# Optimization experiments

Hardware: AMD Instinct MI355X
Metric: run time of the kernel (lower is better)

## Reference

```python
import jax, jax.numpy as jnp
import numpy as np

N_DIMS = 4
NEG_SLOPE = 0.01
ALPHA = 0.5

def leaky(v):
    return jnp.where(v > 0, v, NEG_SLOPE * v)

def gcn_conv(h, W, b, edge_index, n):
    """PyG GCNConv: add self-loops, symmetric normalization, then aggregate."""
    hw = h @ W  # [N, H]
    loops = jnp.arange(n, dtype=edge_index.dtype)
    src = jnp.concatenate([edge_index[0], loops])
    dst = jnp.concatenate([edge_index[1], loops])
    deg = jax.ops.segment_sum(jnp.ones_like(dst, dtype=hw.dtype), dst, num_segments=n)
    dinv = jnp.where(deg > 0, jax.lax.rsqrt(deg), 0.0)
    norm = dinv[src] * dinv[dst]  # [E+N]
    out = jax.ops.segment_sum(hw[src] * norm[:, None], dst, num_segments=n)
    return out + b

def setup_inputs() -> dict:
    key = jax.random.key(0)
    ks = jax.random.split(key, 8)
    N, IN, H, OUT, E = 50000, 512, 256, 512, 800000
    def kaiming(k, shape, fan_in):
        bound = np.sqrt(6.0 / fan_in)  # kaiming_uniform a=sqrt(5)-ish approx; gain sqrt(2)/sqrt(fan_in)*sqrt(3)
        bound = np.sqrt(2.0) * np.sqrt(3.0 / fan_in)
        return jax.random.uniform(k, shape, jnp.float32, -bound, bound)
    x = jax.random.normal(ks[0], (N, IN), jnp.float32)
    all_dim_edge_index = jax.random.randint(ks[1], (N_DIMS, 2, E), 0, N, jnp.int64)
    proj_mat = kaiming(ks[2], (N_DIMS, IN, H), IN)
    gcn_W = jax.random.uniform(ks[3], (N_DIMS, H, H), jnp.float32, -1, 1) * np.sqrt(1.0 / H)
    gcn_b = jnp.zeros((N_DIMS, H), jnp.float32)
    bilinear = kaiming(ks[4], (H, H), H)
    fan = H * N_DIMS
    inv_W = jax.random.uniform(ks[5], (fan, OUT), jnp.float32, -np.sqrt(1.0 / fan), np.sqrt(1.0 / fan))
    inv_b = jax.random.uniform(ks[6], (OUT,), jnp.float32, -np.sqrt(1.0 / fan), np.sqrt(1.0 / fan))
    return {"x": x, "all_dim_edge_index": all_dim_edge_index, "proj_mat": proj_mat,
            "gcn_W": gcn_W, "gcn_b": gcn_b, "bilinear": bilinear, "inv_W": inv_W, "inv_b": inv_b}

def reference(x, all_dim_edge_index, proj_mat, gcn_W, gcn_b, bilinear, inv_W, inv_b):
    n = x.shape[0]
    # per-dimension projection: [n_dims, N, H]
    dim_repr = leaky(jnp.einsum('ni,dih->dnh', x, proj_mat))
    # within-dimension GCN message passing (loop over small fixed n_dims)
    within_aggr = jnp.stack([
        gcn_conv(dim_repr[d], gcn_W[d], gcn_b[d], all_dim_edge_index[d], n)
        for d in range(N_DIMS)])
    # cross-dimension attention
    attention = jnp.einsum('aji,ik,bjk->ab', proj_mat, bilinear, proj_mat)
    attention = jax.nn.softmax(attention, axis=0)
    across_aggr = jnp.einsum('ab,anh->bnh', attention, dim_repr)
    new_dim_repr = ALPHA * within_aggr + (1.0 - ALPHA) * across_aggr  # [n_dims, N, H]
    concat = jnp.transpose(new_dim_repr, (1, 0, 2)).reshape(n, -1)  # [N, n_dims*H]
    return leaky(concat @ inv_W + inv_b)
```

## Files before the change

kernel.cpp:

```cpp
#include <hip/hip_runtime.h>
#include <math.h>

constexpr int N_NODES = 50000;
constexpr int IN_F    = 512;
constexpr int H_F     = 256;
constexpr int OUT_F   = 512;
constexpr int N_EDGE  = 800000;
constexpr int NDIM    = 4;
constexpr long NH     = (long)N_NODES * H_F;

#define LEAKY_SLOPE 0.01f

__device__ __forceinline__ float leaky_f(float v) { return v > 0.0f ? v : LEAKY_SLOPE * v; }

typedef __bf16 bf16x8 __attribute__((ext_vector_type(8)));
typedef float  f32x4  __attribute__((ext_vector_type(4)));

struct PtrTab { const __bf16* h[8]; const __bf16* l[8]; };

__device__ __forceinline__ void gload16(const void* g, void* s) {
  __builtin_amdgcn_global_load_lds(
      (const __attribute__((address_space(1))) void*)g,
      (__attribute__((address_space(3))) void*)s, 16, 0, 0);
}

template<bool AF32>
__global__ __launch_bounds__(256) void gemm_k(
    const float* __restrict__ Af, int ldaf,
    PtrTab at, int lda,
    const __bf16* __restrict__ BhT, const __bf16* __restrict__ BlT, int ldb,
    float* __restrict__ C, int ldc,
    const float* __restrict__ biasVec,
    __bf16* __restrict__ Oh, __bf16* __restrict__ Ol, int ldo,
    int M, int N, int K, int accumulate, int leaky)
{
  __shared__ __bf16 AshF[2][4096];
  __shared__ __bf16 AslF[2][4096];
  __shared__ __bf16 BshF[2][4096];
  __shared__ __bf16 BslF[2][4096];

  const int tid  = threadIdx.x;
  const int lane = tid & 63;
  const int wid  = tid >> 6;
  const int wm   = wid & 1;
  const int wn   = wid >> 1;
  const int l15  = lane & 15;
  const int quad = lane >> 4;

  const int nwg = (int)(gridDim.x * gridDim.y);
  const int hw  = (int)(blockIdx.y * gridDim.x + blockIdx.x);
  const int xcd = hw & 7, idx = hw >> 3;
  const int q8 = nwg >> 3, r8 = nwg & 7;
  const int wk = (xcd < r8 ? xcd * (q8 + 1) : r8 * (q8 + 1) + (xcd - r8) * q8) + idx;
  const int col0 = (wk % (int)gridDim.x) * 128;
  const int row0 = (wk / (int)gridDim.x) * 128;

  f32x4 acc[4][4] = {};
  const int nkt = K >> 5;

  float4 areg[4];

  auto stageB = [&](int buf, int kt) {
    const int kb = kt << 5;
    #pragma unroll
    for (int p = 0; p < 2; ++p) {
      const int c  = tid + p * 256;
      const int rr = c >> 2;
      const int sw = ((c & 3) ^ ((rr >> 1) & 3)) * 8;
      const size_t go = (size_t)(col0 + rr) * ldb + kb + sw;
      gload16(BhT + go, &BshF[buf][c * 8]);
      gload16(BlT + go, &BslF[buf][c * 8]);
    }
  };
  auto stageA = [&](int buf, int kt) {
    const int ch = kt >> 3;
    const __bf16* __restrict__ Ah = at.h[ch];
    const __bf16* __restrict__ Al = at.l[ch];
    const int ka = (kt & 7) << 5;
    #pragma unroll
    for (int p = 0; p < 2; ++p) {
      const int c  = tid + p * 256;
      const int rr = c >> 2;
      const int sw = ((c & 3) ^ ((rr >> 1) & 3)) * 8;
      int row = row0 + rr; row = row < M ? row : M - 1;
      const size_t go = (size_t)row * lda + ka + sw;
      gload16(Ah + go, &AshF[buf][c * 8]);
      gload16(Al + go, &AslF[buf][c * 8]);
    }
  };
  auto loadA32 = [&](int kt) {
    #pragma unroll
    for (int p = 0; p < 4; ++p) {
      const int m = (tid >> 3) + p * 32;
      int row = row0 + m; row = row < M ? row : M - 1;
      areg[p] = *(const float4*)(Af + (size_t)row * ldaf + (kt << 5) + (tid & 7) * 4);
    }
  };
  auto writeA32 = [&](int buf) {
    const int q16 = (tid & 7) >> 1;
    const int sub = (tid & 1) * 4;
    #pragma unroll
    for (int p = 0; p < 4; ++p) {
      const int m = (tid >> 3) + p * 32;
      const float f[4] = {areg[p].x, areg[p].y, areg[p].z, areg[p].w};
      union { __bf16 b[4]; short4 s; } hh, ll;
      #pragma unroll
      for (int i = 0; i < 4; ++i) {
        const __bf16 hb = (__bf16)f[i];
        hh.b[i] = hb;
        ll.b[i] = (__bf16)(f[i] - (float)hb);
      }
      const int off = m * 32 + ((q16 ^ ((m >> 1) & 3)) * 8) + sub;
      *(short4*)&AshF[buf][off] = hh.s;
      *(short4*)&AslF[buf][off] = ll.s;
    }
  };

  if constexpr (AF32) {
    loadA32(0);
    stageB(0, 0);
    writeA32(0);
  } else {
    stageA(0, 0);
    stageB(0, 0);
  }
  __syncthreads();

  int cur = 0;
  for (int kt = 0; kt < nkt; ++kt) {
    const bool more = (kt + 1 < nkt);
    if constexpr (AF32) {
      if (more) { loadA32(kt + 1); stageB(cur ^ 1, kt + 1); }
    } else {
      if (more) { stageA(cur ^ 1, kt + 1); stageB(cur ^ 1, kt + 1); }
    }

    bf16x8 ah[4], al[4], bh[4], bl[4];
    #pragma unroll
    for (int t = 0; t < 4; ++t) {
      const int ar = wm * 64 + t * 16 + l15;
      const int br = wn * 64 + t * 16 + l15;
      const int as = ar * 32 + ((quad ^ ((ar >> 1) & 3)) * 8);
      const int bs = br * 32 + ((quad ^ ((br >> 1) & 3)) * 8);
      ah[t] = *(const bf16x8*)&AshF[cur][as];
      al[t] = *(const bf16x8*)&AslF[cur][as];
      bh[t] = *(const bf16x8*)&BshF[cur][bs];
      bl[t] = *(const bf16x8*)&BslF[cur][bs];
    }
    #pragma unroll
    for (int mt = 0; mt < 4; ++mt)
      #pragma unroll
      for (int nt = 0; nt < 4; ++nt) {
        acc[mt][nt] = __builtin_amdgcn_mfma_f32_16x16x32_bf16(ah[mt], bh[nt], acc[mt][nt], 0, 0, 0);
        acc[mt][nt] = __builtin_amdgcn_mfma_f32_16x16x32_bf16(ah[mt], bl[nt], acc[mt][nt], 0, 0, 0);
        acc[mt][nt] = __builtin_amdgcn_mfma_f32_16x16x32_bf16(al[mt], bh[nt], acc[mt][nt], 0, 0, 0);
      }

    if constexpr (AF32) {
      if (more) writeA32(cur ^ 1);
    }
    __syncthreads();
    cur ^= 1;
  }

  #pragma unroll
  for (int mt = 0; mt < 4; ++mt)
    #pragma unroll
    for (int nt = 0; nt < 4; ++nt) {
      const int col = col0 + wn * 64 + nt * 16 + l15;
      const float bv = biasVec ? biasVec[col] : 0.0f;
      #pragma unroll
      for (int r = 0; r < 4; ++r) {
        const int row = row0 + wm * 64 + mt * 16 + quad * 4 + r;
        if (row < M) {
          float v = acc[mt][nt][r] + bv;
          if (accumulate) v += C[(size_t)row * ldc + col];
          if (leaky) v = leaky_f(v);
          if (Oh) {
            const __bf16 hv = (__bf16)v;
            Oh[(size_t)row * ldo + col] = hv;
            Ol[(size_t)row * ldo + col] = (__bf16)(v - (float)hv);
          } else {
            C[(size_t)row * ldc + col] = v;
          }
        }
      }
    }
}

__global__ void splitT_kernel(const float* __restrict__ B, __bf16* __restrict__ h,
                              __bf16* __restrict__ l, int Kd, int Nd, int total)
{
  int i = blockIdx.x * 256 + threadIdx.x;
  if (i >= total) return;
  int z   = i / (Kd * Nd);
  int rem = i - z * (Kd * Nd);
  int k = rem / Nd;
  int n = rem - k * Nd;
  float v = B[i];
  __bf16 hv = (__bf16)v;
  long o = (long)z * Kd * Nd + (long)n * Kd + k;
  h[o] = hv;
  l[o] = (__bf16)(v - (float)hv);
}

__global__ void splitA_kernel(const float* __restrict__ A, __bf16* __restrict__ h,
                              __bf16* __restrict__ l, long total)
{
  long i = (long)blockIdx.x * 256 + threadIdx.x;
  if (i >= total) return;
  float v = A[i];
  __bf16 hv = (__bf16)v;
  h[i] = hv;
  l[i] = (__bf16)(v - (float)hv);
}

__global__ void bcat_kernel(const float* __restrict__ invW, const float* __restrict__ att,
                            __bf16* __restrict__ h, __bf16* __restrict__ l)
{
  int i = blockIdx.x * 256 + threadIdx.x;
  if (i >= NDIM * OUT_F * 512) return;
  int d   = i >> 18;
  int rem = i & 262143;
  int n = rem >> 9;
  int k = rem & 511;
  float v;
  if (k < H_F) {
    v = invW[(long)(d * H_F + k) * OUT_F + n];
  } else {
    float s = 0.f;
    #pragma unroll
    for (int b = 0; b < 4; ++b)
      s += att[d * 4 + b] * invW[(long)(b * H_F + (k - H_F)) * OUT_F + n];
    v = 0.5f * s;
  }
  __bf16 hv = (__bf16)v;
  long o = (long)n * (NDIM * 512) + d * 512 + k;
  h[o] = hv;
  l[o] = (__bf16)(v - (float)hv);
}

__global__ void deg_count_kernel(const int* __restrict__ edges, int* __restrict__ cnt, int E)
{
  int i = blockIdx.x * 256 + threadIdx.x;
  if (i >= NDIM * E) return;
  int d = i / E;
  int e = i - d * E;
  int t = edges[(long)d * 2 * E + E + e];
  atomicAdd(&cnt[d * N_NODES + t], 1);
}

__global__ __launch_bounds__(1024) void scan_kernel(const int* __restrict__ cnt,
                                                    int* __restrict__ row_start,
                                                    float* __restrict__ dinv)
{
  const int d    = blockIdx.x;
  const int tid  = threadIdx.x;
  const int lane = tid & 63;
  const int wid  = tid >> 6;
  __shared__ int wsum[16];
  __shared__ int carry_s;
  if (tid == 0) carry_s = 0;
  __syncthreads();
  for (int base = 0; base < N_NODES; base += 1024) {
    int i = base + tid;
    int v = (i < N_NODES) ? cnt[d * N_NODES + i] : 0;
    if (i < N_NODES) dinv[d * N_NODES + i] = sqrtf(0.5f / (float)(v + 1));
    int incl = v;
    #pragma unroll
    for (int off = 1; off < 64; off <<= 1) {
      int nb = __shfl_up(incl, off, 64);
      if (lane >= off) incl += nb;
    }
    if (lane == 63) wsum[wid] = incl;
    __syncthreads();
    if (wid == 0 && lane < 16) {
      int s = wsum[lane];
      #pragma unroll
      for (int off = 1; off < 16; off <<= 1) {
        int nb = __shfl_up(s, off, 16);
        if (lane >= off) s += nb;
      }
      wsum[lane] = s;
    }
    __syncthreads();
    int waveoff = (wid == 0) ? 0 : wsum[wid - 1];
    if (i < N_NODES) row_start[d * (N_NODES + 1) + i] = carry_s + waveoff + incl - v;
    __syncthreads();
    if (tid == 1023) carry_s += wsum[15];
    __syncthreads();
  }
  if (tid == 0) row_start[d * (N_NODES + 1) + N_NODES] = carry_s;
}

__global__ void fill_kernel(const int* __restrict__ edges, const int* __restrict__ row_start,
                            int* __restrict__ fill_cnt, int* __restrict__ csr_src, int E)
{
  int i = blockIdx.x * 256 + threadIdx.x;
  if (i >= NDIM * E) return;
  int d = i / E;
  int e = i - d * E;
  int s = edges[(long)d * 2 * E + e];
  int t = edges[(long)d * 2 * E + E + e];
  int pos = row_start[d * (N_NODES + 1) + t] + atomicAdd(&fill_cnt[d * N_NODES + t], 1);
  csr_src[(long)d * E + pos] = s;
}

__global__ __launch_bounds__(256) void gather_aggr_kernel(
    const float* __restrict__ hw, const int* __restrict__ csr_src,
    const int* __restrict__ row_start, const float* __restrict__ dinv,
    const float* __restrict__ bias, __bf16* __restrict__ Wh, __bf16* __restrict__ Wl)
{
  const int n = blockIdx.x * 4 + (threadIdx.x >> 6);
  const int lane = threadIdx.x & 63;
  const float dt = dinv[n];
  const float sl = dt * dt;
  const float4 b = *(const float4*)(bias + lane * 4);
  const float4 h = *(const float4*)(hw + (size_t)n * H_F + lane * 4);
  float4 a0 = make_float4(0.5f * b.x + sl * h.x, 0.5f * b.y + sl * h.y,
                          0.5f * b.z + sl * h.z, 0.5f * b.w + sl * h.w);
  float4 a1 = make_float4(0.f, 0.f, 0.f, 0.f);
  const int beg = row_start[n];
  const int end = row_start[n + 1];
  int j = beg;
  for (; j + 2 <= end; j += 2) {
    const int s0 = csr_src[j];
    const int s1 = csr_src[j + 1];
    const float nm0 = dt * dinv[s0];
    const float nm1 = dt * dinv[s1];
    const float4 v0 = *(const float4*)(hw + (size_t)s0 * H_F + lane * 4);
    const float4 v1 = *(const float4*)(hw + (size_t)s1 * H_F + lane * 4);
    a0.x = fmaf(nm0, v0.x, a0.x); a0.y = fmaf(nm0, v0.y, a0.y);
    a0.z = fmaf(nm0, v0.z, a0.z); a0.w = fmaf(nm0, v0.w, a0.w);
    a1.x = fmaf(nm1, v1.x, a1.x); a1.y = fmaf(nm1, v1.y, a1.y);
    a1.z = fmaf(nm1, v1.z, a1.z); a1.w = fmaf(nm1, v1.w, a1.w);
  }
  if (j < end) {
    const int s0 = csr_src[j];
    const float nm0 = dt * dinv[s0];
    const float4 v0 = *(const float4*)(hw + (size_t)s0 * H_F + lane * 4);
    a0.x = fmaf(nm0, v0.x, a0.x); a0.y = fmaf(nm0, v0.y, a0.y);
    a0.z = fmaf(nm0, v0.z, a0.z); a0.w = fmaf(nm0, v0.w, a0.w);
  }
  const float av[4] = {a0.x + a1.x, a0.y + a1.y, a0.z + a1.z, a0.w + a1.w};
  union { __bf16 b[4]; short4 s; } H, L;
  #pragma unroll
  for (int i = 0; i < 4; ++i) {
    const __bf16 hv = (__bf16)av[i];
    H.b[i] = hv;
    L.b[i] = (__bf16)(av[i] - (float)hv);
  }
  *(short4*)(Wh + (size_t)n * H_F + lane * 4) = H.s;
  *(short4*)(Wl + (size_t)n * H_F + lane * 4) = L.s;
}

__global__ void att_dot_kernel(const float* __restrict__ T, const float* __restrict__ P,
                               float* __restrict__ out16)
{
  const int a = blockIdx.x >> 2;
  const int b = blockIdx.x & 3;
  const float* ta = T + (long)a * (IN_F * H_F);
  const float* pb = P + (long)b * (IN_F * H_F);
  float s = 0.f;
  for (int i = threadIdx.x; i < IN_F * H_F; i += 256) s += ta[i] * pb[i];
  #pragma unroll
  for (int off = 32; off > 0; off >>= 1) s += __shfl_down(s, off, 64);
  __shared__ float red[4];
  if ((threadIdx.x & 63) == 0) red[threadIdx.x >> 6] = s;
  __syncthreads();
  if (threadIdx.x == 0) out16[blockIdx.x] = red[0] + red[1] + red[2] + red[3];
}

__global__ void att_softmax_kernel(const float* __restrict__ raw, float* __restrict__ att)
{
  int b = threadIdx.x;
  if (b < 4) {
    float r0 = raw[b], r1 = raw[4 + b], r2 = raw[8 + b], r3 = raw[12 + b];
    float m = fmaxf(fmaxf(r0, r1), fmaxf(r2, r3));
    float e0 = expf(r0 - m), e1 = expf(r1 - m), e2 = expf(r2 - m), e3 = expf(r3 - m);
    float inv = 1.0f / (e0 + e1 + e2 + e3);
    att[b] = e0 * inv; att[4 + b] = e1 * inv; att[8 + b] = e2 * inv; att[12 + b] = e3 * inv;
  }
}

extern "C" void kernel_launch(void* const* d_in, const int* in_sizes, int n_in,
                              void* d_out, int out_size, void* d_ws, size_t ws_size,
                              hipStream_t stream)
{
  const float* x     = (const float*)d_in[0];
  const int*   edges = (const int*)d_in[1];
  const float* proj  = (const float*)d_in[2];
  const float* gcnW  = (const float*)d_in[3];
  const float* gcnB  = (const float*)d_in[4];
  const float* bil   = (const float*)d_in[5];
  const float* invW  = (const float*)d_in[6];
  const float* invB  = (const float*)d_in[7];
  float* out = (float*)d_out;

  float* HWB       = (float*)d_ws;
  float* dinv      = HWB + NH;
  float* Tbuf      = dinv + NDIM * N_NODES;
  float* att_raw   = Tbuf + (long)NDIM * IN_F * H_F;
  float* att       = att_raw + 16;
  int*   cnt       = (int*)(att + 16);
  int*   fill_cnt  = cnt + NDIM * N_NODES;
  int*   row_start = fill_cnt + NDIM * N_NODES;
  int*   csr_src   = row_start + NDIM * (N_NODES + 1);
  __bf16* projTh   = (__bf16*)(csr_src + (long)NDIM * N_EDGE);
  __bf16* projTl   = projTh + (long)NDIM * IN_F * H_F;
  __bf16* gcnWTh   = projTl + (long)NDIM * IN_F * H_F;
  __bf16* gcnWTl   = gcnWTh + (long)NDIM * H_F * H_F;
  __bf16* bcatTh   = gcnWTl + (long)NDIM * H_F * H_F;
  __bf16* bcatTl   = bcatTh + (long)NDIM * OUT_F * 512;
  __bf16* bilTh    = bcatTl + (long)NDIM * OUT_F * 512;
  __bf16* bilTl    = bilTh + (long)H_F * H_F;
  __bf16* dynBase  = bilTl + (long)H_F * H_F;

  const size_t base_bytes  = (size_t)((char*)dynBase - (char*)d_ws);
  const size_t need_merged = base_bytes + (size_t)16 * NH * sizeof(__bf16);
  const size_t need_xs     = need_merged + (size_t)2 * N_NODES * IN_F * sizeof(__bf16);
  const bool MERGED = ws_size >= need_merged;
  const bool XS     = ws_size >= need_xs;
  const int  RD     = MERGED ? NDIM : 1;

  __bf16* Rh  = dynBase;
  __bf16* Rl  = Rh + (long)RD * NH;
  __bf16* WBh = Rl + (long)RD * NH;
  __bf16* WBl = WBh + (long)RD * NH;
  __bf16* xh  = WBl + (long)RD * NH;
  __bf16* xl  = xh + (long)N_NODES * IN_F;

  const int MBL = (N_NODES + 127) / 128;
  PtrTab empty{};

  hipMemsetAsync(cnt, 0, (size_t)2 * NDIM * N_NODES * sizeof(int), stream);
  deg_count_kernel<<<(NDIM * N_EDGE + 255) / 256, 256, 0, stream>>>(edges, cnt, N_EDGE);
  scan_kernel<<<NDIM, 1024, 0, stream>>>(cnt, row_start, dinv);
  fill_kernel<<<(NDIM * N_EDGE + 255) / 256, 256, 0, stream>>>(edges, row_start, fill_cnt,
                                                               csr_src, N_EDGE);

  splitT_kernel<<<(NDIM * IN_F * H_F + 255) / 256, 256, 0, stream>>>(
      proj, projTh, projTl, IN_F, H_F, NDIM * IN_F * H_F);
  splitT_kernel<<<(NDIM * H_F * H_F + 255) / 256, 256, 0, stream>>>(
      gcnW, gcnWTh, gcnWTl, H_F, H_F, NDIM * H_F * H_F);
  splitT_kernel<<<(H_F * H_F + 255) / 256, 256, 0, stream>>>(
      bil, bilTh, bilTl, H_F, H_F, H_F * H_F);

  for (int a = 0; a < NDIM; ++a)
    gemm_k<true><<<dim3(H_F / 128, IN_F / 128), 256, 0, stream>>>(
        proj + (long)a * IN_F * H_F, H_F,
        empty, 0,
        bilTh, bilTl, H_F,
        Tbuf + (long)a * IN_F * H_F, H_F,
        nullptr, nullptr, nullptr, 0,
        IN_F, H_F, H_F, 0, 0);
  att_dot_kernel<<<16, 256, 0, stream>>>(Tbuf, proj, att_raw);
  att_softmax_kernel<<<1, 64, 0, stream>>>(att_raw, att);
  bcat_kernel<<<(NDIM * OUT_F * 512 + 255) / 256, 256, 0, stream>>>(invW, att, bcatTh, bcatTl);

  if (XS)
    splitA_kernel<<<(int)(((long)N_NODES * IN_F + 255) / 256), 256, 0, stream>>>(
        x, xh, xl, (long)N_NODES * IN_F);

  if (MERGED) {
    for (int d = 0; d < NDIM; ++d) {
      if (XS) {
        PtrTab t{};
        for (int c = 0; c < 8; ++c) { t.h[c] = xh + (c & 1) * 256; t.l[c] = xl + (c & 1) * 256; }
        gemm_k<false><<<dim3(H_F / 128, MBL), 256, 0, stream>>>(
            nullptr, 0, t, IN_F,
            projTh + (long)d * IN_F * H_F, projTl + (long)d * IN_F * H_F, IN_F,
            nullptr, 0, nullptr,
            Rh + (long)d * NH, Rl + (long)d * NH, H_F,
            N_NODES, H_F, IN_F, 0, 1);
      } else {
        gemm_k<true><<<dim3(H_F / 128, MBL), 256, 0, stream>>>(
            x, IN_F, empty, 0,
            projTh + (long)d * IN_F * H_F, projTl + (long)d * IN_F * H_F, IN_F,
            nullptr, 0, nullptr,
            Rh + (long)d * NH, Rl + (long)d * NH, H_F,
            N_NODES, H_F, IN_F, 0, 1);
      }
    }
  }

  for (int d = 0; d < NDIM; ++d) {
    const long rslot = MERGED ? d : 0;
    if (!MERGED) {
      gemm_k<true><<<dim3(H_F / 128, MBL), 256, 0, stream>>>(
          x, IN_F, empty, 0,
          projTh + (long)d * IN_F * H_F, projTl + (long)d * IN_F * H_F, IN_F,
          nullptr, 0, nullptr,
          Rh, Rl, H_F,
          N_NODES, H_F, IN_F, 0, 1);
    }
    {
      PtrTab t{};
      for (int c = 0; c < 8; ++c) { t.h[c] = Rh + rslot * NH; t.l[c] = Rl + rslot * NH; }
      gemm_k<false><<<dim3(H_F / 128, MBL), 256, 0, stream>>>(
          nullptr, 0, t, H_F,
          gcnWTh + (long)d * H_F * H_F, gcnWTl + (long)d * H_F * H_F, H_F,
          HWB, H_F, nullptr,
          nullptr, nullptr, 0,
          N_NODES, H_F, H_F, 0, 0);
    }
    gather_aggr_kernel<<<N_NODES / 4, 256, 0, stream>>>(
        HWB, csr_src + (long)d * N_EDGE, row_start + d * (N_NODES + 1),
        dinv + d * N_NODES, gcnB + d * H_F,
        WBh + rslot * NH, WBl + rslot * NH);

    if (!MERGED) {
      PtrTab t{};
      for (int c = 0; c < 8; ++c) {
        t.h[c] = (c & 1) ? Rh : WBh;
        t.l[c] = (c & 1) ? Rl : WBl;
      }
      gemm_k<false><<<dim3(OUT_F / 128, MBL), 256, 0, stream>>>(
          nullptr, 0, t, H_F,
          bcatTh + (long)d * 512, bcatTl + (long)d * 512, NDIM * 512,
          out, OUT_F, (d == 0) ? invB : nullptr,
          nullptr, nullptr, 0,
          N_NODES, OUT_F, 512, (d == 0) ? 0 : 1, (d == NDIM - 1) ? 1 : 0);
    }
  }

  if (MERGED) {
    PtrTab t{};
    for (int c = 0; c < 8; ++c) {
      const long dd = c >> 1;
      t.h[c] = (c & 1) ? Rh + dd * NH : WBh + dd * NH;
      t.l[c] = (c & 1) ? Rl + dd * NH : WBl + dd * NH;
    }
    gemm_k<false><<<dim3(OUT_F / 128, MBL), 256, 0, stream>>>(
        nullptr, 0, t, H_F,
        bcatTh, bcatTl, NDIM * 512,
        out, OUT_F, invB,
        nullptr, nullptr, 0,
        N_NODES, OUT_F, NDIM * 512, 0, 1);
  }

  (void)in_sizes; (void)n_in; (void)out_size;
}
```

Before: 2.739 ms.

## Pre-tile bf16 operands into MFMA fragment layout and load directly to registers

Introduces a tiled 128x32 block layout for all bf16 hi/lo operands (x, projections, GCN weights, bcat, intermediate activations). A new LDS-free GEMM kernel reads fragments straight from global memory into registers with double buffering, and uses launch bounds for two blocks per CU. The aim is to remove LDS staging, barriers and strided row loads. The workspace plan now uses a flexible fat buffer with several dims per group, and the gather kernel is unrolled to four edges at a time. It trades extra layout-conversion kernels and padded memory for fewer synchronisation and LDS costs, at the risk of less global-load coalescing efficiency.

```diff
diff --git a/kernel.cpp b/kernel.cpp
--- a/kernel.cpp
+++ b/kernel.cpp
@@ -2,6 +2,7 @@
 #include <math.h>
 
 constexpr int N_NODES = 50000;
+constexpr int M_PAD   = 50048;
 constexpr int IN_F    = 512;
 constexpr int H_F     = 256;
 constexpr int OUT_F   = 512;
@@ -16,29 +17,24 @@
 typedef __bf16 bf16x8 __attribute__((ext_vector_type(8)));
 typedef float  f32x4  __attribute__((ext_vector_type(4)));
 
-struct PtrTab { const __bf16* h[8]; const __bf16* l[8]; };
-
-__device__ __forceinline__ void gload16(const void* g, void* s) {
-  __builtin_amdgcn_global_load_lds(
-      (const __attribute__((address_space(1))) void*)g,
-      (__attribute__((address_space(3))) void*)s, 16, 0, 0);
-}
-
-template<bool AF32>
-__global__ __launch_bounds__(256) void gemm_k(
-    const float* __restrict__ Af, int ldaf,
-    PtrTab at, int lda,
-    const __bf16* __restrict__ BhT, const __bf16* __restrict__ BlT, int ldb,
-    float* __restrict__ C, int ldc,
-    const float* __restrict__ biasVec,
-    __bf16* __restrict__ Oh, __bf16* __restrict__ Ol, int ldo,
-    int M, int N, int K, int accumulate, int leaky)
-{
-  __shared__ __bf16 AshF[2][4096];
-  __shared__ __bf16 AslF[2][4096];
-  __shared__ __bf16 BshF[2][4096];
-  __shared__ __bf16 BslF[2][4096];
-
+
+__device__ __forceinline__ void swz_block(int& mb, int& nb) {
+  const int nwg = (int)(gridDim.x * gridDim.y);
+  const int hw  = (int)(blockIdx.y * gridDim.x + blockIdx.x);
+  const int xcd = hw & 7, idx = hw >> 3;
+  const int q8 = nwg >> 3, r8 = nwg & 7;
+  const int wk = (xcd < r8 ? xcd * (q8 + 1) : r8 * (q8 + 1) + (xcd - r8) * q8) + idx;
+  nb = wk % (int)gridDim.x;
+  mb = wk / (int)gridDim.x;
+}
+
+__global__ __launch_bounds__(256, 2) void gemm_s(
+    const __bf16* __restrict__ Ah, const __bf16* __restrict__ Al, int kcTotA, int kcOffA,
+    const __bf16* __restrict__ Bh, const __bf16* __restrict__ Bl, int kcTotB, int kcOffB,
+    float* __restrict__ C, int ldc, const float* __restrict__ biasVec,
+    __bf16* __restrict__ Oh, __bf16* __restrict__ Ol, int kcTotO, int kcOffO,
+    int M, int K, int accumulate, int leaky)
+{
   const int tid  = threadIdx.x;
   const int lane = tid & 63;
   const int wid  = tid >> 6;
@@ -47,17 +43,110 @@
   const int l15  = lane & 15;
   const int quad = lane >> 4;
 
-  const int nwg = (int)(gridDim.x * gridDim.y);
-  const int hw  = (int)(blockIdx.y * gridDim.x + blockIdx.x);
-  const int xcd = hw & 7, idx = hw >> 3;
-  const int q8 = nwg >> 3, r8 = nwg & 7;
-  const int wk = (xcd < r8 ? xcd * (q8 + 1) : r8 * (q8 + 1) + (xcd - r8) * q8) + idx;
-  const int col0 = (wk % (int)gridDim.x) * 128;
-  const int row0 = (wk / (int)gridDim.x) * 128;
+  int mb, nb;
+  swz_block(mb, nb);
+  const int row0 = mb * 128;
+  const int col0 = nb * 128;
+
+  const size_t aB = ((size_t)mb * kcTotA + kcOffA) * 4096 + (size_t)(wm * 64 + l15) * 32 + quad * 8;
+  const size_t bB = ((size_t)nb * kcTotB + kcOffB) * 4096 + (size_t)(wn * 64 + l15) * 32 + quad * 8;
 
   f32x4 acc[4][4] = {};
   const int nkt = K >> 5;
 
+  bf16x8 a0h[4], a0l[4], b0h[4], b0l[4];
+  bf16x8 a1h[4], a1l[4], b1h[4], b1l[4];
+
+  auto load = [&](bf16x8* ah, bf16x8* al, bf16x8* bh, bf16x8* bl, int kt) {
+    const size_t ka = aB + (size_t)kt * 4096;
+    const size_t kb = bB + (size_t)kt * 4096;
+    #pragma unroll
+    for (int t = 0; t < 4; ++t) {
+      ah[t] = *(const bf16x8*)(Ah + ka + t * 512);
+      al[t] = *(const bf16x8*)(Al + ka + t * 512);
+      bh[t] = *(const bf16x8*)(Bh + kb + t * 512);
+      bl[t] = *(const bf16x8*)(Bl + kb + t * 512);
+    }
+  };
+  auto step = [&](bf16x8* ah, bf16x8* al, bf16x8* bh, bf16x8* bl) {
+    #pragma unroll
+    for (int mt = 0; mt < 4; ++mt)
+      #pragma unroll
+      for (int nt = 0; nt < 4; ++nt) {
+        acc[mt][nt] = __builtin_amdgcn_mfma_f32_16x16x32_bf16(ah[mt], bh[nt], acc[mt][nt], 0, 0, 0);
+        acc[mt][nt] = __builtin_amdgcn_mfma_f32_16x16x32_bf16(ah[mt], bl[nt], acc[mt][nt], 0, 0, 0);
+        acc[mt][nt] = __builtin_amdgcn_mfma_f32_16x16x32_bf16(al[mt], bh[nt], acc[mt][nt], 0, 0, 0);
+      }
+  };
+
+  load(a0h, a0l, b0h, b0l, 0);
+  for (int kt = 0; kt < nkt; kt += 2) {
+    load(a1h, a1l, b1h, b1l, kt + 1);
+    step(a0h, a0l, b0h, b0l);
+    if (kt + 2 < nkt) load(a0h, a0l, b0h, b0l, kt + 2);
+    step(a1h, a1l, b1h, b1l);
+  }
+
+  #pragma unroll
+  for (int mt = 0; mt < 4; ++mt)
+    #pragma unroll
+    for (int nt = 0; nt < 4; ++nt) {
+      const int col = col0 + wn * 64 + nt * 16 + l15;
+      const float bv = biasVec ? biasVec[col] : 0.0f;
+      #pragma unroll
+      for (int r = 0; r < 4; ++r) {
+        const int row = row0 + wm * 64 + mt * 16 + quad * 4 + r;
+        if (row < M) {
+          float v = acc[mt][nt][r] + bv;
+          if (accumulate) v += C[(size_t)row * ldc + col];
+          if (leaky) v = leaky_f(v);
+          if (Oh) {
+            const size_t o = ((size_t)mb * kcTotO + kcOffO + (col >> 5)) * 4096
+                           + (size_t)(row & 127) * 32 + (col & 31);
+            const __bf16 hv = (__bf16)v;
+            Oh[o] = hv;
+            Ol[o] = (__bf16)(v - (float)hv);
+          } else {
+            C[(size_t)row * ldc + col] = v;
+          }
+        }
+      }
+    }
+}
+
+__device__ __forceinline__ void gload16(const void* g, void* s) {
+  __builtin_amdgcn_global_load_lds(
+      (const __attribute__((address_space(1))) void*)g,
+      (__attribute__((address_space(3))) void*)s, 16, 0, 0);
+}
+
+__global__ __launch_bounds__(256) void gemm_af32(
+    const float* __restrict__ Af, int ldaf,
+    const __bf16* __restrict__ BhT, const __bf16* __restrict__ BlT, int ldb,
+    float* __restrict__ C, int ldc,
+    __bf16* __restrict__ Oh, __bf16* __restrict__ Ol, int kcTotO, int kcOffO,
+    int M, int K, int leaky)
+{
+  __shared__ __bf16 AshF[2][4096];
+  __shared__ __bf16 AslF[2][4096];
+  __shared__ __bf16 BshF[2][4096];
+  __shared__ __bf16 BslF[2][4096];
+
+  const int tid  = threadIdx.x;
+  const int lane = tid & 63;
+  const int wid  = tid >> 6;
+  const int wm   = wid & 1;
+  const int wn   = wid >> 1;
+  const int l15  = lane & 15;
+  const int quad = lane >> 4;
+
+  int mb, nb;
+  swz_block(mb, nb);
+  const int row0 = mb * 128;
+  const int col0 = nb * 128;
+
+  f32x4 acc[4][4] = {};
+  const int nkt = K >> 5;
   float4 areg[4];
 
   auto stageB = [&](int buf, int kt) {
@@ -70,22 +159,6 @@
       const size_t go = (size_t)(col0 + rr) * ldb + kb + sw;
       gload16(BhT + go, &BshF[buf][c * 8]);
       gload16(BlT + go, &BslF[buf][c * 8]);
-    }
-  };
-  auto stageA = [&](int buf, int kt) {
-    const int ch = kt >> 3;
-    const __bf16* __restrict__ Ah = at.h[ch];
-    const __bf16* __restrict__ Al = at.l[ch];
-    const int ka = (kt & 7) << 5;
-    #pragma unroll
-    for (int p = 0; p < 2; ++p) {
-      const int c  = tid + p * 256;
-      const int rr = c >> 2;
-      const int sw = ((c & 3) ^ ((rr >> 1) & 3)) * 8;
-      int row = row0 + rr; row = row < M ? row : M - 1;
-      const size_t go = (size_t)row * lda + ka + sw;
-      gload16(Ah + go, &AshF[buf][c * 8]);
-      gload16(Al + go, &AslF[buf][c * 8]);
     }
   };
   auto loadA32 = [&](int kt) {
@@ -116,24 +189,15 @@
     }
   };
 
-  if constexpr (AF32) {
-    loadA32(0);
-    stageB(0, 0);
-    writeA32(0);
-  } else {
-    stageA(0, 0);
-    stageB(0, 0);
-  }
+  loadA32(0);
+  stageB(0, 0);
+  writeA32(0);
   __syncthreads();
 
   int cur = 0;
   for (int kt = 0; kt < nkt; ++kt) {
     const bool more = (kt + 1 < nkt);
-    if constexpr (AF32) {
-      if (more) { loadA32(kt + 1); stageB(cur ^ 1, kt + 1); }
-    } else {
-      if (more) { stageA(cur ^ 1, kt + 1); stageB(cur ^ 1, kt + 1); }
-    }
+    if (more) { loadA32(kt + 1); stageB(cur ^ 1, kt + 1); }
 
     bf16x8 ah[4], al[4], bh[4], bl[4];
     #pragma unroll
@@ -156,9 +220,7 @@
         acc[mt][nt] = __builtin_amdgcn_mfma_f32_16x16x32_bf16(al[mt], bh[nt], acc[mt][nt], 0, 0, 0);
       }
 
-    if constexpr (AF32) {
-      if (more) writeA32(cur ^ 1);
-    }
+    if (more) writeA32(cur ^ 1);
     __syncthreads();
     cur ^= 1;
   }
@@ -168,18 +230,18 @@
     #pragma unroll
     for (int nt = 0; nt < 4; ++nt) {
       const int col = col0 + wn * 64 + nt * 16 + l15;
-      const float bv = biasVec ? biasVec[col] : 0.0f;
       #pragma unroll
       for (int r = 0; r < 4; ++r) {
         const int row = row0 + wm * 64 + mt * 16 + quad * 4 + r;
         if (row < M) {
-          float v = acc[mt][nt][r] + bv;
-          if (accumulate) v += C[(size_t)row * ldc + col];
+          float v = acc[mt][nt][r];
           if (leaky) v = leaky_f(v);
           if (Oh) {
+            const size_t o = ((size_t)mb * kcTotO + kcOffO + (col >> 5)) * 4096
+                           + (size_t)(row & 127) * 32 + (col & 31);
             const __bf16 hv = (__bf16)v;
-            Oh[(size_t)row * ldo + col] = hv;
-            Ol[(size_t)row * ldo + col] = (__bf16)(v - (float)hv);
+            Oh[o] = hv;
+            Ol[o] = (__bf16)(v - (float)hv);
           } else {
             C[(size_t)row * ldc + col] = v;
           }
@@ -188,7 +250,24 @@
     }
 }
 
-__global__ void splitT_kernel(const float* __restrict__ B, __bf16* __restrict__ h,
+__global__ void splitTB_tiled(const float* __restrict__ B, __bf16* __restrict__ h,
+                              __bf16* __restrict__ l, int Kd, int Nd, int total)
+{
+  int i = blockIdx.x * 256 + threadIdx.x;
+  if (i >= total) return;
+  int z   = i / (Kd * Nd);
+  int rem = i - z * (Kd * Nd);
+  int k = rem / Nd;
+  int n = rem - k * Nd;
+  float v = B[i];
+  __bf16 hv = (__bf16)v;
+  size_t o = ((size_t)z * (Nd / 128) * (Kd / 32) + (size_t)(n >> 7) * (Kd / 32) + (k >> 5)) * 4096
+           + (size_t)(n & 127) * 32 + (k & 31);
+  h[o] = hv;
+  l[o] = (__bf16)(v - (float)hv);
+}
+
+__global__ void splitT_linear(const float* __restrict__ B, __bf16* __restrict__ h,
                               __bf16* __restrict__ l, int Kd, int Nd, int total)
 {
   int i = blockIdx.x * 256 + threadIdx.x;
@@ -204,19 +283,22 @@
   l[o] = (__bf16)(v - (float)hv);
 }
 
-__global__ void splitA_kernel(const float* __restrict__ A, __bf16* __restrict__ h,
-                              __bf16* __restrict__ l, long total)
+__global__ void splitX_tiled(const float* __restrict__ x, __bf16* __restrict__ h,
+                             __bf16* __restrict__ l)
 {
   long i = (long)blockIdx.x * 256 + threadIdx.x;
-  if (i >= total) return;
-  float v = A[i];
-  __bf16 hv = (__bf16)v;
-  h[i] = hv;
-  l[i] = (__bf16)(v - (float)hv);
-}
-
-__global__ void bcat_kernel(const float* __restrict__ invW, const float* __restrict__ att,
-                            __bf16* __restrict__ h, __bf16* __restrict__ l)
+  if (i >= (long)M_PAD * IN_F) return;
+  const int row = (int)(i >> 9);
+  const int k   = (int)(i & 511);
+  const float v = (row < N_NODES) ? x[(size_t)row * IN_F + k] : 0.0f;
+  const __bf16 hv = (__bf16)v;
+  const size_t o = ((size_t)(row >> 7) * 16 + (k >> 5)) * 4096 + (size_t)(row & 127) * 32 + (k & 31);
+  h[o] = hv;
+  l[o] = (__bf16)(v - (float)hv);
+}
+
+__global__ void bcat_tiled(const float* __restrict__ invW, const float* __restrict__ att,
+                           __bf16* __restrict__ h, __bf16* __restrict__ l)
 {
   int i = blockIdx.x * 256 + threadIdx.x;
   if (i >= NDIM * OUT_F * 512) return;
@@ -235,7 +317,8 @@
     v = 0.5f * s;
   }
   __bf16 hv = (__bf16)v;
-  long o = (long)n * (NDIM * 512) + d * 512 + k;
+  const int kidx = d * 512 + k;
+  const size_t o = ((size_t)(n >> 7) * 64 + (kidx >> 5)) * 4096 + (size_t)(n & 127) * 32 + (kidx & 31);
   h[o] = hv;
   l[o] = (__bf16)(v - (float)hv);
 }
@@ -309,7 +392,8 @@
 __global__ __launch_bounds__(256) void gather_aggr_kernel(
     const float* __restrict__ hw, const int* __restrict__ csr_src,
     const int* __restrict__ row_start, const float* __restrict__ dinv,
-    const float* __restrict__ bias, __bf16* __restrict__ Wh, __bf16* __restrict__ Wl)
+    const float* __restrict__ bias, __bf16* __restrict__ Wh, __bf16* __restrict__ Wl,
+    int kcTotW, int kcOffW)
 {
   const int n = blockIdx.x * 4 + (threadIdx.x >> 6);
   const int lane = threadIdx.x & 63;
@@ -320,29 +404,42 @@
   float4 a0 = make_float4(0.5f * b.x + sl * h.x, 0.5f * b.y + sl * h.y,
                           0.5f * b.z + sl * h.z, 0.5f * b.w + sl * h.w);
   float4 a1 = make_float4(0.f, 0.f, 0.f, 0.f);
+  float4 a2 = make_float4(0.f, 0.f, 0.f, 0.f);
+  float4 a3 = make_float4(0.f, 0.f, 0.f, 0.f);
   const int beg = row_start[n];
   const int end = row_start[n + 1];
   int j = beg;
-  for (; j + 2 <= end; j += 2) {
+  for (; j + 4 <= end; j += 4) {
     const int s0 = csr_src[j];
     const int s1 = csr_src[j + 1];
+    const int s2 = csr_src[j + 2];
+    const int s3 = csr_src[j + 3];
     const float nm0 = dt * dinv[s0];
     const float nm1 = dt * dinv[s1];
+    const float nm2 = dt * dinv[s2];
+    const float nm3 = dt * dinv[s3];
     const float4 v0 = *(const float4*)(hw + (size_t)s0 * H_F + lane * 4);
     const float4 v1 = *(const float4*)(hw + (size_t)s1 * H_F + lane * 4);
+    const float4 v2 = *(const float4*)(hw + (size_t)s2 * H_F + lane * 4);
+    const float4 v3 = *(const float4*)(hw + (size_t)s3 * H_F + lane * 4);
     a0.x = fmaf(nm0, v0.x, a0.x); a0.y = fmaf(nm0, v0.y, a0.y);
     a0.z = fmaf(nm0, v0.z, a0.z); a0.w = fmaf(nm0, v0.w, a0.w);
     a1.x = fmaf(nm1, v1.x, a1.x); a1.y = fmaf(nm1, v1.y, a1.y);
     a1.z = fmaf(nm1, v1.z, a1.z); a1.w = fmaf(nm1, v1.w, a1.w);
-  }
-  if (j < end) {
+    a2.x = fmaf(nm2, v2.x, a2.x); a2.y = fmaf(nm2, v2.y, a2.y);
+    a2.z = fmaf(nm2, v2.z, a2.z); a2.w = fmaf(nm2, v2.w, a2.w);
+    a3.x = fmaf(nm3, v3.x, a3.x); a3.y = fmaf(nm3, v3.y, a3.y);
+    a3.z = fmaf(nm3, v3.z, a3.z); a3.w = fmaf(nm3, v3.w, a3.w);
+  }
+  for (; j < end; ++j) {
     const int s0 = csr_src[j];
     const float nm0 = dt * dinv[s0];
     const float4 v0 = *(const float4*)(hw + (size_t)s0 * H_F + lane * 4);
     a0.x = fmaf(nm0, v0.x, a0.x); a0.y = fmaf(nm0, v0.y, a0.y);
     a0.z = fmaf(nm0, v0.z, a0.z); a0.w = fmaf(nm0, v0.w, a0.w);
   }
-  const float av[4] = {a0.x + a1.x, a0.y + a1.y, a0.z + a1.z, a0.w + a1.w};
+  const float av[4] = {a0.x + a1.x + a2.x + a3.x, a0.y + a1.y + a2.y + a3.y,
+                       a0.z + a1.z + a2.z + a3.z, a0.w + a1.w + a2.w + a3.w};
   union { __bf16 b[4]; short4 s; } H, L;
   #pragma unroll
   for (int i = 0; i < 4; ++i) {
@@ -350,8 +447,10 @@
     H.b[i] = hv;
     L.b[i] = (__bf16)(av[i] - (float)hv);
   }
-  *(short4*)(Wh + (size_t)n * H_F + lane * 4) = H.s;
-  *(short4*)(Wl + (size_t)n * H_F + lane * 4) = L.s;
+  const size_t o = ((size_t)(n >> 7) * kcTotW + kcOffW + (lane >> 3)) * 4096
+                 + (size_t)(n & 127) * 32 + (lane & 7) * 4;
+  *(short4*)(Wh + o) = H.s;
+  *(short4*)(Wl + o) = L.s;
 }
 
 __global__ void att_dot_kernel(const float* __restrict__ T, const float* __restrict__ P,
@@ -406,32 +505,36 @@
   int*   fill_cnt  = cnt + NDIM * N_NODES;
   int*   row_start = fill_cnt + NDIM * N_NODES;
   int*   csr_src   = row_start + NDIM * (N_NODES + 1);
-  __bf16* projTh   = (__bf16*)(csr_src + (long)NDIM * N_EDGE);
-  __bf16* projTl   = projTh + (long)NDIM * IN_F * H_F;
-  __bf16* gcnWTh   = projTl + (long)NDIM * IN_F * H_F;
-  __bf16* gcnWTl   = gcnWTh + (long)NDIM * H_F * H_F;
-  __bf16* bcatTh   = gcnWTl + (long)NDIM * H_F * H_F;
-  __bf16* bcatTl   = bcatTh + (long)NDIM * OUT_F * 512;
-  __bf16* bilTh    = bcatTl + (long)NDIM * OUT_F * 512;
-  __bf16* bilTl    = bilTh + (long)H_F * H_F;
-  __bf16* dynBase  = bilTl + (long)H_F * H_F;
-
-  const size_t base_bytes  = (size_t)((char*)dynBase - (char*)d_ws);
-  const size_t need_merged = base_bytes + (size_t)16 * NH * sizeof(__bf16);
-  const size_t need_xs     = need_merged + (size_t)2 * N_NODES * IN_F * sizeof(__bf16);
-  const bool MERGED = ws_size >= need_merged;
-  const bool XS     = ws_size >= need_xs;
-  const int  RD     = MERGED ? NDIM : 1;
-
-  __bf16* Rh  = dynBase;
-  __bf16* Rl  = Rh + (long)RD * NH;
-  __bf16* WBh = Rl + (long)RD * NH;
-  __bf16* WBl = WBh + (long)RD * NH;
-  __bf16* xh  = WBl + (long)RD * NH;
-  __bf16* xl  = xh + (long)N_NODES * IN_F;
-
-  const int MBL = (N_NODES + 127) / 128;
-  PtrTab empty{};
+  __bf16* projLinH = (__bf16*)(csr_src + (long)NDIM * N_EDGE);
+  __bf16* projLinL = projLinH + (long)NDIM * IN_F * H_F;
+  __bf16* bilLinH  = projLinL + (long)NDIM * IN_F * H_F;
+  __bf16* bilLinL  = bilLinH + (long)H_F * H_F;
+  __bf16* projTBh  = bilLinL + (long)H_F * H_F;
+  __bf16* projTBl  = projTBh + (long)NDIM * 32 * 4096;
+  __bf16* gcnWTBh  = projTBl + (long)NDIM * 32 * 4096;
+  __bf16* gcnWTBl  = gcnWTBh + (long)NDIM * 16 * 4096;
+  __bf16* bcatTBh  = gcnWTBl + (long)NDIM * 16 * 4096;
+  __bf16* bcatTBl  = bcatTBh + (long)4 * 64 * 4096;
+  __bf16* dynBase  = bcatTBl + (long)4 * 64 * 4096;
+
+  const size_t base_bytes = (size_t)((char*)dynBase - (char*)d_ws);
+  auto fatBytes = [](int ktot) { return (size_t)2 * 391 * (ktot / 32) * 4096 * sizeof(__bf16); };
+  const size_t xBytes = (size_t)2 * 391 * 16 * 4096 * sizeof(__bf16);
+  int KTOT; bool XS;
+  if      (ws_size >= base_bytes + fatBytes(2048) + xBytes) { KTOT = 2048; XS = true;  }
+  else if (ws_size >= base_bytes + fatBytes(1024) + xBytes) { KTOT = 1024; XS = true;  }
+  else if (ws_size >= base_bytes + fatBytes(512)  + xBytes) { KTOT = 512;  XS = true;  }
+  else                                                      { KTOT = 512;  XS = false; }
+  const int DPG  = KTOT / 512;
+  const int NGEN = NDIM / DPG;
+  const int KC   = KTOT / 32;
+
+  __bf16* fatH = dynBase;
+  __bf16* fatL = fatH + (size_t)391 * KC * 4096;
+  __bf16* xh   = fatL + (size_t)391 * KC * 4096;
+  __bf16* xl   = xh + (size_t)391 * 16 * 4096;
+
+  const int MBL = 391;
 
   hipMemsetAsync(cnt, 0, (size_t)2 * NDIM * N_NODES * sizeof(int), stream);
   deg_count_kernel<<<(NDIM * N_EDGE + 255) / 256, 256, 0, stream>>>(edges, cnt, N_EDGE);
@@ -439,104 +542,68 @@
   fill_kernel<<<(NDIM * N_EDGE + 255) / 256, 256, 0, stream>>>(edges, row_start, fill_cnt,
                                                                csr_src, N_EDGE);
 
-  splitT_kernel<<<(NDIM * IN_F * H_F + 255) / 256, 256, 0, stream>>>(
-      proj, projTh, projTl, IN_F, H_F, NDIM * IN_F * H_F);
-  splitT_kernel<<<(NDIM * H_F * H_F + 255) / 256, 256, 0, stream>>>(
-      gcnW, gcnWTh, gcnWTl, H_F, H_F, NDIM * H_F * H_F);
-  splitT_kernel<<<(H_F * H_F + 255) / 256, 256, 0, stream>>>(
-      bil, bilTh, bilTl, H_F, H_F, H_F * H_F);
+  splitT_linear<<<(NDIM * IN_F * H_F + 255) / 256, 256, 0, stream>>>(
+      proj, projLinH, projLinL, IN_F, H_F, NDIM * IN_F * H_F);
+  splitT_linear<<<(H_F * H_F + 255) / 256, 256, 0, stream>>>(
+      bil, bilLinH, bilLinL, H_F, H_F, H_F * H_F);
+  splitTB_tiled<<<(NDIM * IN_F * H_F + 255) / 256, 256, 0, stream>>>(
+      proj, projTBh, projTBl, IN_F, H_F, NDIM * IN_F * H_F);
+  splitTB_tiled<<<(NDIM * H_F * H_F + 255) / 256, 256, 0, stream>>>(
+      gcnW, gcnWTBh, gcnWTBl, H_F, H_F, NDIM * H_F * H_F);
 
   for (int a = 0; a < NDIM; ++a)
-    gemm_k<true><<<dim3(H_F / 128, IN_F / 128), 256, 0, stream>>>(
+    gemm_af32<<<dim3(H_F / 128, IN_F / 128), 256, 0, stream>>>(
         proj + (long)a * IN_F * H_F, H_F,
-        empty, 0,
-        bilTh, bilTl, H_F,
+        bilLinH, bilLinL, H_F,
         Tbuf + (long)a * IN_F * H_F, H_F,
-        nullptr, nullptr, nullptr, 0,
-        IN_F, H_F, H_F, 0, 0);
+        nullptr, nullptr, 0, 0,
+        IN_F, H_F, 0);
   att_dot_kernel<<<16, 256, 0, stream>>>(Tbuf, proj, att_raw);
   att_softmax_kernel<<<1, 64, 0, stream>>>(att_raw, att);
-  bcat_kernel<<<(NDIM * OUT_F * 512 + 255) / 256, 256, 0, stream>>>(invW, att, bcatTh, bcatTl);
+  bcat_tiled<<<(NDIM * OUT_F * 512 + 255) / 256, 256, 0, stream>>>(invW, att, bcatTBh, bcatTBl);
 
   if (XS)
-    splitA_kernel<<<(int)(((long)N_NODES * IN_F + 255) / 256), 256, 0, stream>>>(
-        x, xh, xl, (long)N_NODES * IN_F);
-
-  if (MERGED) {
-    for (int d = 0; d < NDIM; ++d) {
-      if (XS) {
-        PtrTab t{};
-        for (int c = 0; c < 8; ++c) { t.h[c] = xh + (c & 1) * 256; t.l[c] = xl + (c & 1) * 256; }
-        gemm_k<false><<<dim3(H_F / 128, MBL), 256, 0, stream>>>(
-            nullptr, 0, t, IN_F,
-            projTh + (long)d * IN_F * H_F, projTl + (long)d * IN_F * H_F, IN_F,
+    splitX_tiled<<<(int)(((long)M_PAD * IN_F + 255) / 256), 256, 0, stream>>>(x, xh, xl);
+
+  for (int g = 0; g < NGEN; ++g) {
+    for (int j = 0; j < DPG; ++j) {
+      const int d   = g * DPG + j;
+      const int kcW = j * 16;
+      const int kcR = j * 16 + 8;
+
+      if (XS)
+        gemm_s<<<dim3(H_F / 128, MBL), 256, 0, stream>>>(
+            xh, xl, 16, 0,
+            projTBh + (size_t)d * 32 * 4096, projTBl + (size_t)d * 32 * 4096, 16, 0,
             nullptr, 0, nullptr,
-            Rh + (long)d * NH, Rl + (long)d * NH, H_F,
-            N_NODES, H_F, IN_F, 0, 1);
-      } else {
-        gemm_k<true><<<dim3(H_F / 128, MBL), 256, 0, stream>>>(
-            x, IN_F, empty, 0,
-            projTh + (long)d * IN_F * H_F, projTl + (long)d * IN_F * H_F, IN_F,
-            nullptr, 0, nullptr,
-            Rh + (long)d * NH, Rl + (long)d * NH, H_F,
-            N_NODES, H_F, IN_F, 0, 1);
-      }
-    }
-  }
-
-  for (int d = 0; d < NDIM; ++d) {
-    const long rslot = MERGED ? d : 0;
-    if (!MERGED) {
-      gemm_k<true><<<dim3(H_F / 128, MBL), 256, 0, stream>>>(
-          x, IN_F, empty, 0,
-          projTh + (long)d * IN_F * H_F, projTl + (long)d * IN_F * H_F, IN_F,
-          nullptr, 0, nullptr,
-          Rh, Rl, H_F,
-          N_NODES, H_F, IN_F, 0, 1);
-    }
-    {
-      PtrTab t{};
-      for (int c = 0; c < 8; ++c) { t.h[c] = Rh + rslot * NH; t.l[c] = Rl + rslot * NH; }
-      gemm_k<false><<<dim3(H_F / 128, MBL), 256, 0, stream>>>(
-          nullptr, 0, t, H_F,
-          gcnWTh + (long)d * H_F * H_F, gcnWTl + (long)d * H_F * H_F, H_F,
+            fatH, fatL, KC, kcR,
+            N_NODES, IN_F, 0, 1);
+      else
+        gemm_af32<<<dim3(H_F / 128, MBL), 256, 0, stream>>>(
+            x, IN_F,
+            projLinH + (long)d * IN_F * H_F, projLinL + (long)d * IN_F * H_F, IN_F,
+            nullptr, 0,
+            fatH, fatL, KC, kcR,
+            N_NODES, IN_F, 1);
+
+      gemm_s<<<dim3(H_F / 128, MBL), 256, 0, stream>>>(
+          fatH, fatL, KC, kcR,
+          gcnWTBh + (size_t)d * 16 * 4096, gcnWTBl + (size_t)d * 16 * 4096, 8, 0,
           HWB, H_F, nullptr,
-          nullptr, nullptr, 0,
-          N_NODES, H_F, H_F, 0, 0);
-    }
-    gather_aggr_kernel<<<N_NODES / 4, 256, 0, stream>>>(
-        HWB, csr_src + (long)d * N_EDGE, row_start + d * (N_NODES + 1),
-        dinv + d * N_NODES, gcnB + d * H_F,
-        WBh + rslot * NH, WBl + rslot * NH);
-
-    if (!MERGED) {
-      PtrTab t{};
-      for (int c = 0; c < 8; ++c) {
-        t.h[c] = (c & 1) ? Rh : WBh;
-        t.l[c] = (c & 1) ? Rl : WBl;
-      }
-      gemm_k<false><<<dim3(OUT_F / 128, MBL), 256, 0, stream>>>(
-          nullptr, 0, t, H_F,
-          bcatTh + (long)d * 512, bcatTl + (long)d * 512, NDIM * 512,
-          out, OUT_F, (d == 0) ? invB : nullptr,
-          nullptr, nullptr, 0,
-          N_NODES, OUT_F, 512, (d == 0) ? 0 : 1, (d == NDIM - 1) ? 1 : 0);
-    }
-  }
-
-  if (MERGED) {
-    PtrTab t{};
-    for (int c = 0; c < 8; ++c) {
-      const long dd = c >> 1;
-      t.h[c] = (c & 1) ? Rh + dd * NH : WBh + dd * NH;
-      t.l[c] = (c & 1) ? Rl + dd * NH : WBl + dd * NH;
-    }
-    gemm_k<false><<<dim3(OUT_F / 128, MBL), 256, 0, stream>>>(
-        nullptr, 0, t, H_F,
-        bcatTh, bcatTl, NDIM * 512,
-        out, OUT_F, invB,
-        nullptr, nullptr, 0,
-        N_NODES, OUT_F, NDIM * 512, 0, 1);
+          nullptr, nullptr, 0, 0,
+          N_NODES, H_F, 0, 0);
+
+      gather_aggr_kernel<<<N_NODES / 4, 256, 0, stream>>>(
+          HWB, csr_src + (long)d * N_EDGE, row_start + d * (N_NODES + 1),
+          dinv + d * N_NODES, gcnB + d * H_F, fatH, fatL, KC, kcW);
+    }
+
+    gemm_s<<<dim3(OUT_F / 128, MBL), 256, 0, stream>>>(
+        fatH, fatL, KC, 0,
+        bcatTBh, bcatTBl, 64, g * DPG * 16,
+        out, OUT_F, (g == 0) ? invB : nullptr,
+        nullptr, nullptr, 0, 0,
+        N_NODES, KTOT, (g == 0) ? 0 : 1, (g == NGEN - 1) ? 1 : 0);
   }
 
   (void)in_sizes; (void)n_in; (void)out_size;
```

Result: faster. 2.541 ms (-7.2%).
